# Kernel tuning notes

Hardware: AMD Instinct MI355X
Metric: run time of the kernel (lower is better)

Reference implementation:

```python
import jax, jax.numpy as jnp
import numpy as np

B, D, L = 16384, 2048, 6

def setup_inputs() -> dict:
    key = jax.random.key(0)
    kx, kw = jax.random.split(key)
    x = jax.random.normal(kx, (B, D), dtype=jnp.float32)
    # cross weights: xavier_normal on (D,1) -> std = sqrt(2/(D+1)); stacked [L, D]
    std = float(np.sqrt(2.0 / (D + 1)))
    W = jax.random.normal(kw, (L, D), dtype=jnp.float32) * std
    b = jnp.zeros((L, D), dtype=jnp.float32)  # bias params init to zeros
    return {"x": x, "W": W, "b": b}

def reference(x, W, b):
    # Original per layer: x_l = (x0 @ x_l^T) @ w_i + b_i + x_l
    # Algebraically identical: x_l = x0 * (x_l . w_i) + b_i + x_l  (scalar per row)
    x_l = x
    for i in range(W.shape[0]):
        s = jnp.einsum('bd,d->b', x_l, W[i])          # [B]
        x_l = x * s[:, None] + b[i][None, :] + x_l     # [B, D]
    return x_l
```

## Files before the change

kernel.cpp:

```cpp
#include <hip/hip_runtime.h>

#define B_ROWS   16384
#define D_DIM    2048
#define L_LAYERS 6
#define THREADS  512
#define BLOCKS   1024
#define WPB      (THREADS / 64)
#define ROWS_PER_WAVE 2

__global__ __launch_bounds__(THREADS) void cross_net_kernel(
    const float* __restrict__ x,
    const float* __restrict__ W,
    const float* __restrict__ b,
    float* __restrict__ out)
{
    __shared__ float Wl[L_LAYERS][D_DIM];
    __shared__ float Ul[D_DIM];
    __shared__ float red[WPB][L_LAYERS];

    const int t    = threadIdx.x;
    const int lane = t & 63;
    const int wid  = t >> 6;

    {
        const int base = t * 4;
        float4 prefix = make_float4(0.f, 0.f, 0.f, 0.f);
        float e_red[L_LAYERS];
        #pragma unroll
        for (int l = 0; l < L_LAYERS; ++l) {
            const float4 wv = *(const float4*)(W + l * D_DIM + base);
            const float4 bv = *(const float4*)(b + l * D_DIM + base);
            e_red[l] = prefix.x * wv.x + prefix.y * wv.y +
                       prefix.z * wv.z + prefix.w * wv.w;
            prefix.x += bv.x; prefix.y += bv.y; prefix.z += bv.z; prefix.w += bv.w;
            *(float4*)&Wl[l][base] = wv;
        }
        *(float4*)&Ul[base] = prefix;
        #pragma unroll
        for (int l = 0; l < L_LAYERS; ++l) {
            float v = e_red[l];
            #pragma unroll
            for (int off = 32; off >= 1; off >>= 1) v += __shfl_xor(v, off, 64);
            if (lane == 0) red[wid][l] = v;
        }
    }
    __syncthreads();

    float e[L_LAYERS];
    #pragma unroll
    for (int l = 0; l < L_LAYERS; ++l) {
        float s = 0.f;
        #pragma unroll
        for (int w = 0; w < WPB; ++w) s += red[w][l];
        e[l] = s;
    }

    const int gw   = blockIdx.x * WPB + wid;
    const int row0 = gw * ROWS_PER_WAVE;
    const float* xr0 = x + (size_t)row0 * D_DIM;
    const float* xr1 = xr0 + D_DIM;
    const int eoff = lane * 4;

    float4 xa[8], xb[8];
    #pragma unroll
    for (int j = 0; j < 8; ++j) xa[j] = *(const float4*)(xr0 + j * 256 + eoff);
    #pragma unroll
    for (int j = 0; j < 8; ++j) xb[j] = *(const float4*)(xr1 + j * 256 + eoff);

    float p0[L_LAYERS], p1[L_LAYERS];
    #pragma unroll
    for (int l = 0; l < L_LAYERS; ++l) {
        float a0 = 0.f, a1 = 0.f;
        #pragma unroll
        for (int j = 0; j < 8; ++j) {
            const float4 wv = *(const float4*)&Wl[l][j * 256 + eoff];
            a0 += xa[j].x * wv.x + xa[j].y * wv.y + xa[j].z * wv.z + xa[j].w * wv.w;
            a1 += xb[j].x * wv.x + xb[j].y * wv.y + xb[j].z * wv.z + xb[j].w * wv.w;
        }
        p0[l] = a0; p1[l] = a1;
    }

    #pragma unroll
    for (int off = 32; off >= 1; off >>= 1) {
        #pragma unroll
        for (int l = 0; l < L_LAYERS; ++l) {
            p0[l] += __shfl_xor(p0[l], off, 64);
            p1[l] += __shfl_xor(p1[l], off, 64);
        }
    }

    float c0 = 1.f, c1 = 1.f;
    #pragma unroll
    for (int l = 0; l < L_LAYERS; ++l) {
        c0 = c0 * (1.f + p0[l]) + e[l];
        c1 = c1 * (1.f + p1[l]) + e[l];
    }

    float* or0 = out + (size_t)row0 * D_DIM;
    float* or1 = or0 + D_DIM;
    #pragma unroll
    for (int j = 0; j < 8; ++j) {
        const float4 uv = *(const float4*)&Ul[j * 256 + eoff];
        float4 o0, o1;
        o0.x = c0 * xa[j].x + uv.x; o0.y = c0 * xa[j].y + uv.y;
        o0.z = c0 * xa[j].z + uv.z; o0.w = c0 * xa[j].w + uv.w;
        o1.x = c1 * xb[j].x + uv.x; o1.y = c1 * xb[j].y + uv.y;
        o1.z = c1 * xb[j].z + uv.z; o1.w = c1 * xb[j].w + uv.w;
        *(float4*)(or0 + j * 256 + eoff) = o0;
        *(float4*)(or1 + j * 256 + eoff) = o1;
    }
}

extern "C" void kernel_launch(void* const* d_in, const int* in_sizes, int n_in,
                              void* d_out, int out_size, void* d_ws, size_t ws_size,
                              hipStream_t stream) {
    (void)in_sizes; (void)n_in; (void)d_ws; (void)ws_size; (void)out_size;
    const float* x = (const float*)d_in[0];
    const float* W = (const float*)d_in[1];
    const float* b = (const float*)d_in[2];
    float* out = (float*)d_out;
    cross_net_kernel<<<dim3(BLOCKS), dim3(THREADS), 0, stream>>>(x, W, b, out);
}
```

Measured before the change: 242.8 us.

## Process four rows per wave with software-pipelined prefetch of next row

Halves the grid and has each wave handle four rows in sequence, loading the next row into registers while the current row is reduced and written. This amortises the per-block prologue (W/b staging into LDS and the bias-term reduction) over twice as many rows and overlaps global loads with compute. In exchange there are fewer blocks in flight (512 on a large GPU), less memory-level parallelism per wave than loading both rows at once, and the serial row loop may leave load latency exposed.

```diff
diff --git a/kernel.cpp b/kernel.cpp
--- a/kernel.cpp
+++ b/kernel.cpp
@@ -4,9 +4,9 @@
 #define D_DIM    2048
 #define L_LAYERS 6
 #define THREADS  512
-#define BLOCKS   1024
+#define BLOCKS   512
 #define WPB      (THREADS / 64)
-#define ROWS_PER_WAVE 2
+#define ROWS_PER_WAVE 4
 
 __global__ __launch_bounds__(THREADS) void cross_net_kernel(
     const float* __restrict__ x,
@@ -57,57 +57,60 @@
 
     const int gw   = blockIdx.x * WPB + wid;
     const int row0 = gw * ROWS_PER_WAVE;
-    const float* xr0 = x + (size_t)row0 * D_DIM;
-    const float* xr1 = xr0 + D_DIM;
+    const float* xr  = x   + (size_t)row0 * D_DIM;
+    float*       orw = out + (size_t)row0 * D_DIM;
     const int eoff = lane * 4;
 
-    float4 xa[8], xb[8];
+    float4 cur[8], nxt[8];
     #pragma unroll
-    for (int j = 0; j < 8; ++j) xa[j] = *(const float4*)(xr0 + j * 256 + eoff);
+    for (int j = 0; j < 8; ++j) cur[j] = *(const float4*)(xr + j * 256 + eoff);
+
     #pragma unroll
-    for (int j = 0; j < 8; ++j) xb[j] = *(const float4*)(xr1 + j * 256 + eoff);
+    for (int r = 0; r < ROWS_PER_WAVE; ++r) {
+        if (r < ROWS_PER_WAVE - 1) {
+            const float* xn = xr + D_DIM;
+            #pragma unroll
+            for (int j = 0; j < 8; ++j) nxt[j] = *(const float4*)(xn + j * 256 + eoff);
+        }
 
-    float p0[L_LAYERS], p1[L_LAYERS];
-    #pragma unroll
-    for (int l = 0; l < L_LAYERS; ++l) {
-        float a0 = 0.f, a1 = 0.f;
+        float p[L_LAYERS];
+        #pragma unroll
+        for (int l = 0; l < L_LAYERS; ++l) {
+            float a = 0.f;
+            #pragma unroll
+            for (int j = 0; j < 8; ++j) {
+                const float4 wv = *(const float4*)&Wl[l][j * 256 + eoff];
+                a += cur[j].x * wv.x + cur[j].y * wv.y +
+                     cur[j].z * wv.z + cur[j].w * wv.w;
+            }
+            p[l] = a;
+        }
+
+        #pragma unroll
+        for (int off = 32; off >= 1; off >>= 1) {
+            #pragma unroll
+            for (int l = 0; l < L_LAYERS; ++l) p[l] += __shfl_xor(p[l], off, 64);
+        }
+
+        float c = 1.f;
+        #pragma unroll
+        for (int l = 0; l < L_LAYERS; ++l) c = c * (1.f + p[l]) + e[l];
+
         #pragma unroll
         for (int j = 0; j < 8; ++j) {
-            const float4 wv = *(const float4*)&Wl[l][j * 256 + eoff];
-            a0 += xa[j].x * wv.x + xa[j].y * wv.y + xa[j].z * wv.z + xa[j].w * wv.w;
-            a1 += xb[j].x * wv.x + xb[j].y * wv.y + xb[j].z * wv.z + xb[j].w * wv.w;
+            const float4 uv = *(const float4*)&Ul[j * 256 + eoff];
+            float4 o;
+            o.x = c * cur[j].x + uv.x; o.y = c * cur[j].y + uv.y;
+            o.z = c * cur[j].z + uv.z; o.w = c * cur[j].w + uv.w;
+            *(float4*)(orw + j * 256 + eoff) = o;
         }
-        p0[l] = a0; p1[l] = a1;
-    }
 
-    #pragma unroll
-    for (int off = 32; off >= 1; off >>= 1) {
-        #pragma unroll
-        for (int l = 0; l < L_LAYERS; ++l) {
-            p0[l] += __shfl_xor(p0[l], off, 64);
-            p1[l] += __shfl_xor(p1[l], off, 64);
+        xr  += D_DIM;
+        orw += D_DIM;
+        if (r < ROWS_PER_WAVE - 1) {
+            #pragma unroll
+            for (int j = 0; j < 8; ++j) cur[j] = nxt[j];
         }
-    }
-
-    float c0 = 1.f, c1 = 1.f;
-    #pragma unroll
-    for (int l = 0; l < L_LAYERS; ++l) {
-        c0 = c0 * (1.f + p0[l]) + e[l];
-        c1 = c1 * (1.f + p1[l]) + e[l];
-    }
-
-    float* or0 = out + (size_t)row0 * D_DIM;
-    float* or1 = or0 + D_DIM;
-    #pragma unroll
-    for (int j = 0; j < 8; ++j) {
-        const float4 uv = *(const float4*)&Ul[j * 256 + eoff];
-        float4 o0, o1;
-        o0.x = c0 * xa[j].x + uv.x; o0.y = c0 * xa[j].y + uv.y;
-        o0.z = c0 * xa[j].z + uv.z; o0.w = c0 * xa[j].w + uv.w;
-        o1.x = c1 * xb[j].x + uv.x; o1.y = c1 * xb[j].y + uv.y;
-        o1.z = c1 * xb[j].z + uv.z; o1.w = c1 * xb[j].w + uv.w;
-        *(float4*)(or0 + j * 256 + eoff) = o0;
-        *(float4*)(or1 + j * 256 + eoff) = o1;
     }
 }
 
```

New measurement: 372.8 us. 53.5% more time.
